# Kernel optimization log

Hardware: AMD Instinct MI355X
Metric: run time of the kernel (lower is better)

## Reference

```python
import jax, jax.numpy as jnp
import numpy as np
from jax.scipy.special import logsumexp

EPS = 0.001
MAX_ITER = 100
LOG_EPS = 1e-8


def _M(C, u, v):
    # M_ij = (-c_ij + u_i + v_j) / eps ; shapes: C (N,P1,P2), u (N,P1), v (N,P2)
    return (-C + u[..., :, None] + v[..., None, :]) / EPS


def setup_inputs() -> dict:
    key = jax.random.key(0)
    k1, k2, k3 = jax.random.split(key, 3)
    N, P1, P2 = 16, 1024, 1024
    mu = jax.random.uniform(k1, (N, P1), dtype=jnp.float32)
    nu = jax.random.uniform(k2, (N, P2), dtype=jnp.float32)
    C = jax.random.uniform(k3, (N, P1, P2), dtype=jnp.float32)
    return {"mu": mu, "nu": nu, "C": C}


def reference(mu, nu, C):
    log_mu = jnp.log(mu + LOG_EPS)
    log_nu = jnp.log(nu + LOG_EPS)
    u0 = jnp.ones_like(mu)
    v0 = jnp.ones_like(nu)

    def body(carry, _):
        u, v = carry
        # logsumexp over P1 axis (transpose(-2,-1) then dim=-1 in torch == axis=-2)
        v = EPS * (log_nu - logsumexp(_M(C, u, v), axis=-2)) + v
        u = EPS * (log_mu - logsumexp(_M(C, u, v), axis=-1)) + u
        return (u, v), None

    (u, v), _ = jax.lax.scan(body, (u0, v0), None, length=MAX_ITER)
    pi = jax.lax.stop_gradient(jnp.exp(_M(C, u, v)))
    cost = jnp.sum(pi * C, axis=(-2, -1))
    return cost, pi
```

## Files before the change

### kernel.cpp

```cpp
#include <hip/hip_runtime.h>
#include <math.h>

#define NB 16
#define P 1024
#define EPSV 1e-3f
#define INV_EPS 1000.0f
#define LOGEPS 1e-8f
#define ITERS 100
#define NBLK 256
#define SPB (NB * 16 * P)

__device__ __forceinline__ void cstore(float* p, float v) {
  __hip_atomic_store(p, v, __ATOMIC_RELAXED, __HIP_MEMORY_SCOPE_AGENT);
}

__device__ __forceinline__ void load_psum16(const float* ps, int voff, float* x) {
  const float* b0 = ps + 1 * P;   const float* b1 = ps + 3 * P;
  const float* b2 = ps + 5 * P;   const float* b3 = ps + 7 * P;
  const float* b4 = ps + 9 * P;   const float* b5 = ps + 11 * P;
  const float* b6 = ps + 13 * P;  const float* b7 = ps + 15 * P;
  asm volatile(
      "global_load_dword %0, %16, %17 offset:-4096 sc0 sc1\n\t"
      "global_load_dword %1, %16, %17 sc0 sc1\n\t"
      "global_load_dword %2, %16, %18 offset:-4096 sc0 sc1\n\t"
      "global_load_dword %3, %16, %18 sc0 sc1\n\t"
      "global_load_dword %4, %16, %19 offset:-4096 sc0 sc1\n\t"
      "global_load_dword %5, %16, %19 sc0 sc1\n\t"
      "global_load_dword %6, %16, %20 offset:-4096 sc0 sc1\n\t"
      "global_load_dword %7, %16, %20 sc0 sc1\n\t"
      "global_load_dword %8, %16, %21 offset:-4096 sc0 sc1\n\t"
      "global_load_dword %9, %16, %21 sc0 sc1\n\t"
      "global_load_dword %10, %16, %22 offset:-4096 sc0 sc1\n\t"
      "global_load_dword %11, %16, %22 sc0 sc1\n\t"
      "global_load_dword %12, %16, %23 offset:-4096 sc0 sc1\n\t"
      "global_load_dword %13, %16, %23 sc0 sc1\n\t"
      "global_load_dword %14, %16, %24 offset:-4096 sc0 sc1\n\t"
      "global_load_dword %15, %16, %24 sc0 sc1\n\t"
      "s_waitcnt vmcnt(0)"
      : "=v"(x[0]), "=v"(x[1]), "=v"(x[2]), "=v"(x[3]),
        "=v"(x[4]), "=v"(x[5]), "=v"(x[6]), "=v"(x[7]),
        "=v"(x[8]), "=v"(x[9]), "=v"(x[10]), "=v"(x[11]),
        "=v"(x[12]), "=v"(x[13]), "=v"(x[14]), "=v"(x[15])
      : "v"(voff), "s"(b0), "s"(b1), "s"(b2), "s"(b3),
        "s"(b4), "s"(b5), "s"(b6), "s"(b7)
      : "memory");
}

__global__ void __launch_bounds__(1024)
sink_k(const float* __restrict__ C, const float* __restrict__ mu,
       const float* __restrict__ nu, float* __restrict__ out,
       float* __restrict__ psum, int* __restrict__ bar) {
  const int tid = threadIdx.x;
  const int blk = blockIdx.x;
  const int n = (blk & 7) * 2 + ((blk >> 3) >> 4);
  const int rb = (blk >> 3) & 15;
  const int wv = tid >> 6, ln = tid & 63;
  const int r0 = rb * 64 + wv * 4;
  const int c0 = ln * 16;

  __shared__ float ssum[P];
  __shared__ float vsh[P];
  __shared__ float bsh[P];
  __shared__ float red[16];

  float E[4][16];
  const float* Cn = C + (size_t)n * P * P;
#pragma unroll
  for (int r = 0; r < 4; ++r) {
#pragma unroll
    for (int k = 0; k < 16; k += 4) {
      float4 c4 = *(const float4*)(Cn + (size_t)(r0 + r) * P + c0 + k);
      E[r][k]     = __expf(-c4.x * INV_EPS);
      E[r][k + 1] = __expf(-c4.y * INV_EPS);
      E[r][k + 2] = __expf(-c4.z * INV_EPS);
      E[r][k + 3] = __expf(-c4.w * INV_EPS);
    }
  }
  float elmu[4];
#pragma unroll
  for (int r = 0; r < 4; ++r) elmu[r] = EPSV * __logf(mu[n * P + r0 + r] + LOGEPS);
  const int cv = ln * 16 + wv;
  const float elnu_cv = EPSV * __logf(nu[n * P + cv] + LOGEPS);

  float a[4] = {1.0f, 1.0f, 1.0f, 1.0f};
  float u[4];
  int* bcnt = bar + n * 32;
  ssum[tid] = 0.0f;
  __syncthreads();

  for (int it = 0; it < ITERS; ++it) {
    const int par = it & 1;
#pragma unroll
    for (int k = 0; k < 16; ++k) {
      float val = a[0] * E[0][k];
      val = __fmaf_rn(a[1], E[1][k], val);
      val = __fmaf_rn(a[2], E[2][k], val);
      val = __fmaf_rn(a[3], E[3][k], val);
      atomicAdd(&ssum[k * 64 + ln], val);
    }
    __syncthreads();
    float Sv = ssum[tid];
    cstore(&psum[(size_t)par * SPB + (size_t)(n * 16 + rb) * P + tid], Sv);
    ssum[tid] = 0.0f;
    asm volatile("s_waitcnt vmcnt(0)" ::: "memory");
    __syncthreads();

    if (tid == 0) {
      __hip_atomic_fetch_add(bcnt, 1, __ATOMIC_RELAXED, __HIP_MEMORY_SCOPE_AGENT);
      const int target = (it + 1) * 16;
      while (__hip_atomic_load(bcnt, __ATOMIC_RELAXED, __HIP_MEMORY_SCOPE_AGENT) < target)
        __builtin_amdgcn_s_sleep(1);
    }
    __syncthreads();

    float sp[16];
    load_psum16(psum + (size_t)par * SPB + (size_t)n * 16 * P, tid * 4, sp);
    float S = (sp[0] + sp[1]) + (sp[2] + sp[3]);
    S += (sp[4] + sp[5]) + (sp[6] + sp[7]);
    S += (sp[8] + sp[9]) + (sp[10] + sp[11]);
    S += (sp[12] + sp[13]) + (sp[14] + sp[15]);
    float v_cv = elnu_cv - 1.0f - EPSV * __logf(S);
    vsh[tid] = v_cv;
    bsh[tid] = __expf((v_cv + 1.0f) * INV_EPS);
    __syncthreads();

    float T[4] = {0.0f, 0.0f, 0.0f, 0.0f};
#pragma unroll
    for (int k = 0; k < 16; ++k) {
      float b = bsh[k * 64 + ln];
      T[0] = __fmaf_rn(E[0][k], b, T[0]);
      T[1] = __fmaf_rn(E[1][k], b, T[1]);
      T[2] = __fmaf_rn(E[2][k], b, T[2]);
      T[3] = __fmaf_rn(E[3][k], b, T[3]);
    }
#pragma unroll
    for (int off = 1; off < 64; off <<= 1) {
      T[0] += __shfl_xor(T[0], off);
      T[1] += __shfl_xor(T[1], off);
      T[2] += __shfl_xor(T[2], off);
      T[3] += __shfl_xor(T[3], off);
    }
#pragma unroll
    for (int r = 0; r < 4; ++r) {
      u[r] = elmu[r] + 1.0f - EPSV * __logf(T[r]);
      a[r] = __expf((u[r] - 1.0f) * INV_EPS);
    }
  }

  float acc = 0.0f;
  float* pi = out + 16 + (size_t)n * P * P;
#pragma unroll
  for (int r = 0; r < 4; ++r) {
    const float* Cr = Cn + (size_t)(r0 + r) * P + c0;
    float* pr = pi + (size_t)(r0 + r) * P + c0;
#pragma unroll
    for (int k = 0; k < 16; k += 4) {
      float4 c4 = *(const float4*)(Cr + k);
      float4 pv;
      pv.x = __expf((u[r] + vsh[(k + 0) * 64 + ln] - c4.x) * INV_EPS);
      pv.y = __expf((u[r] + vsh[(k + 1) * 64 + ln] - c4.y) * INV_EPS);
      pv.z = __expf((u[r] + vsh[(k + 2) * 64 + ln] - c4.z) * INV_EPS);
      pv.w = __expf((u[r] + vsh[(k + 3) * 64 + ln] - c4.w) * INV_EPS);
      *(float4*)(pr + k) = pv;
      acc = __fmaf_rn(pv.x, c4.x, acc);
      acc = __fmaf_rn(pv.y, c4.y, acc);
      acc = __fmaf_rn(pv.z, c4.z, acc);
      acc = __fmaf_rn(pv.w, c4.w, acc);
    }
  }
#pragma unroll
  for (int off = 1; off < 64; off <<= 1) acc += __shfl_xor(acc, off);
  __syncthreads();
  if (ln == 0) red[wv] = acc;
  __syncthreads();
  if (tid == 0) {
    float t = 0.0f;
#pragma unroll
    for (int w = 0; w < 16; ++w) t += red[w];
    atomicAdd(out + n, t);
  }
}

extern "C" void kernel_launch(void* const* d_in, const int* in_sizes, int n_in,
                              void* d_out, int out_size, void* d_ws, size_t ws_size,
                              hipStream_t stream) {
  const float* mu = (const float*)d_in[0];
  const float* nu = (const float*)d_in[1];
  const float* C  = (const float*)d_in[2];
  float* out = (float*)d_out;
  float* ws = (float*)d_ws;

  float* psum = ws;
  int* bar    = (int*)(ws + 2 * SPB);

  hipMemsetAsync(out, 0, NB * sizeof(float), stream);
  hipMemsetAsync(bar, 0, NB * 32 * sizeof(int), stream);

  void* args[] = {(void*)&C, (void*)&mu, (void*)&nu, (void*)&out,
                  (void*)&psum, (void*)&bar};
  hipLaunchCooperativeKernel((const void*)sink_k, dim3(NBLK), dim3(1024),
                             args, 0, stream);
}
```

Baseline: 2.594 ms.

## Replace atomic counter grid barrier with tagged value-flag pair polling

Each block now publishes its partial column sums as 64-bit (value, iteration tag) pairs with a single atomic store. Consumer threads poll the exact pairs they need until every tag matches the current iteration. This removes the per-iteration counter atomic, the single-thread spin, a store-drain wait and two block-wide syncs. The cost is doubled workspace traffic per iteration and repeated polling loads from every thread. Correctness relies on tags increasing monotonically in each parity buffer, and on whatever the workspace holds before the first launch not matching the tags the first iterations wait for.

```diff
diff --git a/kernel.cpp b/kernel.cpp
--- a/kernel.cpp
+++ b/kernel.cpp
@@ -8,39 +8,34 @@
 #define LOGEPS 1e-8f
 #define ITERS 100
 #define NBLK 256
-#define SPB (NB * 16 * P)
-
-__device__ __forceinline__ void cstore(float* p, float v) {
-  __hip_atomic_store(p, v, __ATOMIC_RELAXED, __HIP_MEMORY_SCOPE_AGENT);
-}
-
-__device__ __forceinline__ void load_psum16(const float* ps, int voff, float* x) {
-  const float* b0 = ps + 1 * P;   const float* b1 = ps + 3 * P;
-  const float* b2 = ps + 5 * P;   const float* b3 = ps + 7 * P;
-  const float* b4 = ps + 9 * P;   const float* b5 = ps + 11 * P;
-  const float* b6 = ps + 13 * P;  const float* b7 = ps + 15 * P;
+#define PPB (NB * 16 * P * 2)
+
+typedef float v2f __attribute__((ext_vector_type(2)));
+
+__device__ __forceinline__ void publish_pair(float* p, float S, float tag) {
+  union { float2 f; unsigned long long u; } x;
+  x.f.x = S; x.f.y = tag;
+  __hip_atomic_store((unsigned long long*)p, x.u, __ATOMIC_RELAXED,
+                     __HIP_MEMORY_SCOPE_AGENT);
+}
+
+__device__ __forceinline__ void load_pairs8(
+    const float* b0, const float* b1, const float* b2, const float* b3,
+    const float* b4, const float* b5, const float* b6, const float* b7,
+    int voff, v2f& p0, v2f& p1, v2f& p2, v2f& p3,
+    v2f& p4, v2f& p5, v2f& p6, v2f& p7) {
   asm volatile(
-      "global_load_dword %0, %16, %17 offset:-4096 sc0 sc1\n\t"
-      "global_load_dword %1, %16, %17 sc0 sc1\n\t"
-      "global_load_dword %2, %16, %18 offset:-4096 sc0 sc1\n\t"
-      "global_load_dword %3, %16, %18 sc0 sc1\n\t"
-      "global_load_dword %4, %16, %19 offset:-4096 sc0 sc1\n\t"
-      "global_load_dword %5, %16, %19 sc0 sc1\n\t"
-      "global_load_dword %6, %16, %20 offset:-4096 sc0 sc1\n\t"
-      "global_load_dword %7, %16, %20 sc0 sc1\n\t"
-      "global_load_dword %8, %16, %21 offset:-4096 sc0 sc1\n\t"
-      "global_load_dword %9, %16, %21 sc0 sc1\n\t"
-      "global_load_dword %10, %16, %22 offset:-4096 sc0 sc1\n\t"
-      "global_load_dword %11, %16, %22 sc0 sc1\n\t"
-      "global_load_dword %12, %16, %23 offset:-4096 sc0 sc1\n\t"
-      "global_load_dword %13, %16, %23 sc0 sc1\n\t"
-      "global_load_dword %14, %16, %24 offset:-4096 sc0 sc1\n\t"
-      "global_load_dword %15, %16, %24 sc0 sc1\n\t"
+      "global_load_dwordx2 %0, %8, %9 sc0 sc1\n\t"
+      "global_load_dwordx2 %1, %8, %10 sc0 sc1\n\t"
+      "global_load_dwordx2 %2, %8, %11 sc0 sc1\n\t"
+      "global_load_dwordx2 %3, %8, %12 sc0 sc1\n\t"
+      "global_load_dwordx2 %4, %8, %13 sc0 sc1\n\t"
+      "global_load_dwordx2 %5, %8, %14 sc0 sc1\n\t"
+      "global_load_dwordx2 %6, %8, %15 sc0 sc1\n\t"
+      "global_load_dwordx2 %7, %8, %16 sc0 sc1\n\t"
       "s_waitcnt vmcnt(0)"
-      : "=v"(x[0]), "=v"(x[1]), "=v"(x[2]), "=v"(x[3]),
-        "=v"(x[4]), "=v"(x[5]), "=v"(x[6]), "=v"(x[7]),
-        "=v"(x[8]), "=v"(x[9]), "=v"(x[10]), "=v"(x[11]),
-        "=v"(x[12]), "=v"(x[13]), "=v"(x[14]), "=v"(x[15])
+      : "=v"(p0), "=v"(p1), "=v"(p2), "=v"(p3),
+        "=v"(p4), "=v"(p5), "=v"(p6), "=v"(p7)
       : "v"(voff), "s"(b0), "s"(b1), "s"(b2), "s"(b3),
         "s"(b4), "s"(b5), "s"(b6), "s"(b7)
       : "memory");
@@ -49,7 +44,7 @@
 __global__ void __launch_bounds__(1024)
 sink_k(const float* __restrict__ C, const float* __restrict__ mu,
        const float* __restrict__ nu, float* __restrict__ out,
-       float* __restrict__ psum, int* __restrict__ bar) {
+       float* __restrict__ psum2) {
   const int tid = threadIdx.x;
   const int blk = blockIdx.x;
   const int n = (blk & 7) * 2 + ((blk >> 3) >> 4);
@@ -84,12 +79,12 @@
 
   float a[4] = {1.0f, 1.0f, 1.0f, 1.0f};
   float u[4];
-  int* bcnt = bar + n * 32;
   ssum[tid] = 0.0f;
   __syncthreads();
 
   for (int it = 0; it < ITERS; ++it) {
     const int par = it & 1;
+    const float want = (float)(it + 1);
 #pragma unroll
     for (int k = 0; k < 16; ++k) {
       float val = a[0] * E[0][k];
@@ -100,25 +95,40 @@
     }
     __syncthreads();
     float Sv = ssum[tid];
-    cstore(&psum[(size_t)par * SPB + (size_t)(n * 16 + rb) * P + tid], Sv);
+    publish_pair(psum2 + ((size_t)((par * NB + n) * 16 + rb) * P + tid) * 2,
+                 Sv, want);
     ssum[tid] = 0.0f;
-    asm volatile("s_waitcnt vmcnt(0)" ::: "memory");
-    __syncthreads();
-
-    if (tid == 0) {
-      __hip_atomic_fetch_add(bcnt, 1, __ATOMIC_RELAXED, __HIP_MEMORY_SCOPE_AGENT);
-      const int target = (it + 1) * 16;
-      while (__hip_atomic_load(bcnt, __ATOMIC_RELAXED, __HIP_MEMORY_SCOPE_AGENT) < target)
+
+    const float* pb = psum2 + (size_t)(par * NB + n) * 16 * P * 2;
+    const int voff = tid * 8;
+    float S = 0.0f;
+    {
+      v2f p0, p1, p2, p3, p4, p5, p6, p7;
+      for (;;) {
+        load_pairs8(pb, pb + 2 * P, pb + 4 * P, pb + 6 * P,
+                    pb + 8 * P, pb + 10 * P, pb + 12 * P, pb + 14 * P,
+                    voff, p0, p1, p2, p3, p4, p5, p6, p7);
+        if (p0.y == want && p1.y == want && p2.y == want && p3.y == want &&
+            p4.y == want && p5.y == want && p6.y == want && p7.y == want)
+          break;
         __builtin_amdgcn_s_sleep(1);
-    }
-    __syncthreads();
-
-    float sp[16];
-    load_psum16(psum + (size_t)par * SPB + (size_t)n * 16 * P, tid * 4, sp);
-    float S = (sp[0] + sp[1]) + (sp[2] + sp[3]);
-    S += (sp[4] + sp[5]) + (sp[6] + sp[7]);
-    S += (sp[8] + sp[9]) + (sp[10] + sp[11]);
-    S += (sp[12] + sp[13]) + (sp[14] + sp[15]);
+      }
+      S += ((p0.x + p1.x) + (p2.x + p3.x)) + ((p4.x + p5.x) + (p6.x + p7.x));
+    }
+    {
+      const float* qb = pb + 16 * P;
+      v2f p0, p1, p2, p3, p4, p5, p6, p7;
+      for (;;) {
+        load_pairs8(qb, qb + 2 * P, qb + 4 * P, qb + 6 * P,
+                    qb + 8 * P, qb + 10 * P, qb + 12 * P, qb + 14 * P,
+                    voff, p0, p1, p2, p3, p4, p5, p6, p7);
+        if (p0.y == want && p1.y == want && p2.y == want && p3.y == want &&
+            p4.y == want && p5.y == want && p6.y == want && p7.y == want)
+          break;
+        __builtin_amdgcn_s_sleep(1);
+      }
+      S += ((p0.x + p1.x) + (p2.x + p3.x)) + ((p4.x + p5.x) + (p6.x + p7.x));
+    }
     float v_cv = elnu_cv - 1.0f - EPSV * __logf(S);
     vsh[tid] = v_cv;
     bsh[tid] = __expf((v_cv + 1.0f) * INV_EPS);
@@ -188,16 +198,11 @@
   const float* nu = (const float*)d_in[1];
   const float* C  = (const float*)d_in[2];
   float* out = (float*)d_out;
-  float* ws = (float*)d_ws;
-
-  float* psum = ws;
-  int* bar    = (int*)(ws + 2 * SPB);
+  float* psum2 = (float*)d_ws;
 
   hipMemsetAsync(out, 0, NB * sizeof(float), stream);
-  hipMemsetAsync(bar, 0, NB * 32 * sizeof(int), stream);
-
-  void* args[] = {(void*)&C, (void*)&mu, (void*)&nu, (void*)&out,
-                  (void*)&psum, (void*)&bar};
+
+  void* args[] = {(void*)&C, (void*)&mu, (void*)&nu, (void*)&out, (void*)&psum2};
   hipLaunchCooperativeKernel((const void*)sink_k, dim3(NBLK), dim3(1024),
                              args, 0, stream);
 }
```

After: 3.074 ms. +18.5%, slower.
